# Performance work log

Measured on AMD Instinct MI355X. Metric: run time of the kernel, lower is better.

The kernel has to match this reference:

```python
import jax, jax.numpy as jnp
import numpy as np

DIM = 512
HEADS = 8
HEAD_DIM = DIM // HEADS
KS = 5


def setup_inputs() -> dict:
    key = jax.random.key(0)
    ks = jax.random.split(key, 6)
    B, H, W = 4, 128, 128
    N, C = H * W, DIM
    x = jax.random.normal(ks[0], (B, N, C), jnp.float32)
    Wq = jax.random.normal(ks[1], (C, C), jnp.float32) * 0.02
    bq = jnp.zeros((C,), jnp.float32)
    Wkv = jax.random.normal(ks[2], (2 * C, C), jnp.float32) * 0.02
    bkv = jnp.zeros((2 * C,), jnp.float32)
    Wp = jax.random.normal(ks[3], (C, C), jnp.float32) * 0.02
    bp = jnp.zeros((C,), jnp.float32)
    focusing_factor = jnp.ones((C,), jnp.float32) * 3.0
    scale = jnp.zeros((C,), jnp.float32)
    dwc_w = jax.random.normal(ks[4], (HEAD_DIM, 1, KS, KS), jnp.float32) * np.sqrt(2.0 / (KS * KS)).astype(np.float32)
    dwc_b = jnp.zeros((HEAD_DIM,), jnp.float32)
    return {"x": x, "Wq": Wq, "bq": bq, "Wkv": Wkv, "bkv": bkv, "Wp": Wp, "bp": bp,
            "focusing_factor": focusing_factor, "scale": scale, "dwc_w": dwc_w, "dwc_b": dwc_b,
            "H": H, "W": W}


def reference(x, Wq, bq, Wkv, bkv, Wp, bp, focusing_factor, scale, dwc_w, dwc_b, H, W):
    B, N, C = x.shape
    h, d = HEADS, C // HEADS
    q = x @ Wq.T + bq
    kv = x @ Wkv.T + bkv
    k, v = kv[..., :C], kv[..., C:]
    s = jax.nn.softplus(scale)
    q = (jax.nn.relu(q) + 1e-6) / s
    k = (jax.nn.relu(k) + 1e-6) / s
    q_norm = jnp.linalg.norm(q, axis=-1, keepdims=True)
    k_norm = jnp.linalg.norm(k, axis=-1, keepdims=True)
    q = q ** focusing_factor
    k = k ** focusing_factor
    q = q / jnp.linalg.norm(q, axis=-1, keepdims=True) * q_norm
    k = k / jnp.linalg.norm(k, axis=-1, keepdims=True) * k_norm
    # [B, h, N, d]
    q = q.reshape(B, N, h, d).transpose(0, 2, 1, 3)
    k = k.reshape(B, N, h, d).transpose(0, 2, 1, 3)
    v = v.reshape(B, N, h, d).transpose(0, 2, 1, 3)
    n = N
    k_mean = k.mean(axis=2)  # [B, h, d]
    z = 1.0 / (jnp.einsum('bhnd,bhd->bhn', q, k_mean) + 1e-6)  # [B, h, N]
    inv_sqrt_n = n ** (-0.5)
    kv_mat = jnp.einsum('bhnd,bhne->bhde', k * inv_sqrt_n, v * inv_sqrt_n)  # [B, h, d, d]
    attn = jnp.einsum('bhnd,bhde->bhne', q, kv_mat) * z[..., None]  # [B, h, N, d]
    x_attn = attn.transpose(0, 2, 1, 3).reshape(B, N, C)
    # depthwise conv branch on v, per (batch*head) image of shape [d, H, W]
    v_img = v.reshape(B * h, H, W, d).transpose(0, 3, 1, 2)
    pad = KS // 2
    conv = jax.lax.conv_general_dilated(v_img, dwc_w, (1, 1), [(pad, pad), (pad, pad)],
                                        feature_group_count=d,
                                        dimension_numbers=('NCHW', 'OIHW', 'NCHW'))
    conv = conv + dwc_b[None, :, None, None]
    x_conv = conv.reshape(B, C, N).transpose(0, 2, 1)
    return (x_attn + x_conv) @ Wp.T + bp
```

## Files before the change

### kernel.cpp

```cpp
#include <hip/hip_runtime.h>
#include <cstdio>

#define N_TOK 16384
#define CDIM  512

typedef unsigned short ushort_t;
typedef _Float16 f16;
typedef __attribute__((ext_vector_type(8))) _Float16 f16x8;
typedef __attribute__((ext_vector_type(4))) _Float16 f16x4;
typedef __attribute__((ext_vector_type(4))) float f32x4;

__device__ __forceinline__ float fast_pow(float x, float p) {
  return __builtin_amdgcn_exp2f(p * __builtin_amdgcn_logf(x));
}
__device__ __forceinline__ void gl_lds16(const void* g, void* l) {
  __builtin_amdgcn_global_load_lds((const __attribute__((address_space(1))) void*)g,
                                   (__attribute__((address_space(3))) void*)l, 16, 0, 0);
}
__device__ __forceinline__ int perm_col(int k, int r) {
  const int kg = k >> 5, c8 = (k >> 3) & 3, e = k & 7;
  return kg * 32 + ((c8 ^ ((r >> 1) & 3)) * 8) + e;
}

__global__ void zero_kernel(float* __restrict__ p, int n) {
  int i = blockIdx.x * blockDim.x + threadIdx.x;
  if (i < n) p[i] = 0.f;
}

__global__ void sp_kernel(const float* __restrict__ scale, float* __restrict__ inv_s) {
  int i = blockIdx.x * blockDim.x + threadIdx.x;
  if (i < 512) {
    float sc = scale[i];
    float s = (sc > 20.f) ? sc : log1pf(expf(sc));
    inv_s[i] = 1.0f / s;
  }
}

__global__ __launch_bounds__(256) void cvt_perm_kernel(const float* __restrict__ in,
                                                       f16* __restrict__ out, int n4) {
  int i = blockIdx.x * blockDim.x + threadIdx.x;
  const int stride = gridDim.x * blockDim.x;
  for (; i < n4; i += stride) {
    float4 v = ((const float4*)in)[i];
    const int r = i >> 7;
    const int f = i & 127;
    const int kg = f >> 3;
    const int c = (f >> 1) & 3;
    const int e = (f & 1) * 4;
    const int dst = r * 512 + kg * 32 + ((c ^ ((r >> 1) & 3)) * 8) + e;
    f16x4 h;
    h.x = (f16)v.x; h.y = (f16)v.y; h.z = (f16)v.z; h.w = (f16)v.w;
    *(f16x4*)&out[dst] = h;
  }
}

template <int OUT16>
__global__ __launch_bounds__(256, 4) void gemm_f16(const f16* __restrict__ A,
                                                   const f16* __restrict__ Bw,
                                                   const float* __restrict__ b1,
                                                   const float* __restrict__ b2,
                                                   float* __restrict__ C32,
                                                   f16* __restrict__ C16,
                                                   const int K, const int nY,
                                                   const int ncol1, const int ldc) {
  __shared__ __align__(16) f16 SMEM[16896];
  const int t = threadIdx.x;
  const int lane = t & 63;
  const int w = t >> 6;
  const int wr = w >> 1, wc = w & 1;

  const int id = blockIdx.x;
  const int xcd = id & 7;
  const int j = id >> 3;
  const int xpc = (int)(gridDim.x) / (nY * 8);
  const int xloc = j / nY;
  const int y = j - xloc * nY;
  const size_t bm = (size_t)(xcd * xpc + xloc) * 128;
  const int bn = y * 128;

  const int lr = lane & 15;
  const int ksl = lane >> 4;

  f32x4 acc[4][4] = {};

  auto stage = [&](int k0, int buf) {
    const int rsub = lane >> 2;
    const int csub = (lane & 3) * 8;
    const size_t ga = (bm + w * 32 + rsub) * (size_t)K + k0 + csub;
    const size_t gb = ((size_t)(bn + w * 32 + rsub)) * K + k0 + csub;
    f16* Ab = SMEM + buf * 4096;
    f16* Bb = SMEM + 8192 + buf * 4096;
    gl_lds16(A + ga,                   Ab + (w * 32) * 32);
    gl_lds16(A + ga + 16 * (size_t)K,  Ab + (w * 32 + 16) * 32);
    gl_lds16(Bw + gb,                  Bb + (w * 32) * 32);
    gl_lds16(Bw + gb + 16 * (size_t)K, Bb + (w * 32 + 16) * 32);
  };

  const int nsteps = K >> 5;
  stage(0, 0);
  for (int s = 0; s < nsteps; ++s) {
    const int buf = s & 1;
    __syncthreads();
    const f16* Ab = SMEM + buf * 4096;
    const f16* Bb = SMEM + 8192 + buf * 4096;
    f16x8 a[4], b[4];
#pragma unroll
    for (int i = 0; i < 4; ++i) {
      const int rA = wr * 64 + i * 16 + lr;
      a[i] = *(const f16x8*)&Ab[rA * 32 + ((ksl ^ ((rA >> 1) & 3)) * 8)];
      const int rB = wc * 64 + i * 16 + lr;
      b[i] = *(const f16x8*)&Bb[rB * 32 + ((ksl ^ ((rB >> 1) & 3)) * 8)];
    }
    if (s + 1 < nsteps) stage((s + 1) << 5, buf ^ 1);
#pragma unroll
    for (int mi = 0; mi < 4; ++mi)
#pragma unroll
      for (int ni = 0; ni < 4; ++ni)
        acc[mi][ni] = __builtin_amdgcn_mfma_f32_16x16x32_f16(a[mi], b[ni], acc[mi][ni], 0, 0, 0);
  }

  const int rg = (lane >> 4) << 2;
  if (OUT16) {
    __syncthreads();
#pragma unroll
    for (int ni = 0; ni < 4; ++ni) {
      const int cl = wc * 64 + ni * 16 + lr;
      const int cg = bn + cl;
      const float bs = (cg < ncol1) ? b1[cg] : b2[cg - ncol1];
#pragma unroll
      for (int mi = 0; mi < 4; ++mi)
#pragma unroll
        for (int j2 = 0; j2 < 4; ++j2)
          SMEM[(wr * 64 + mi * 16 + rg + j2) * 132 + cl] = (f16)(acc[mi][ni][j2] + bs);
    }
    __syncthreads();
#pragma unroll
    for (int i = 0; i < 8; ++i) {
      const int idx = i * 256 + t;
      const int rl = idx >> 4, ch = (idx & 15) * 8;
      *(f16x8*)&C16[(bm + rl) * (size_t)ldc + bn + ch] = *(const f16x8*)&SMEM[rl * 132 + ch];
    }
  } else {
#pragma unroll
    for (int ni = 0; ni < 4; ++ni) {
      const int col = bn + wc * 64 + ni * 16 + lr;
      const float bs = (col < ncol1) ? b1[col] : b2[col - ncol1];
#pragma unroll
      for (int mi = 0; mi < 4; ++mi) {
        float* Cp = C32 + (bm + wr * 64 + mi * 16 + rg) * (size_t)ldc + col;
#pragma unroll
        for (int j2 = 0; j2 < 4; ++j2)
          Cp[(size_t)j2 * ldc] = acc[mi][ni][j2] + bs;
      }
    }
  }
}

__global__ __launch_bounds__(256) void nonlin16_kernel(f16* __restrict__ qkv,
                                                       const float* __restrict__ inv_s,
                                                       const float* __restrict__ ff) {
  const int t = threadIdx.x, lane = t & 63, w = t >> 6;
  const int row = blockIdx.x * 4 + w;
  f16* qr = qkv + (size_t)row * 1536 + lane * 8;
  f16* kr = qr + 512;
  f16x8 qh = *(const f16x8*)qr;
  f16x8 kh = *(const f16x8*)kr;
  float is[8], fv[8];
  *(float4*)&is[0] = *(const float4*)(inv_s + lane * 8);
  *(float4*)&is[4] = *(const float4*)(inv_s + lane * 8 + 4);
  *(float4*)&fv[0] = *(const float4*)(ff + lane * 8);
  *(float4*)&fv[4] = *(const float4*)(ff + lane * 8 + 4);

  float qv[8], kval[8], sq = 0.f, sk = 0.f;
#pragma unroll
  for (int i = 0; i < 8; ++i) {
    qv[i] = (fmaxf((float)qh[i], 0.f) + 1e-6f) * is[i];
    kval[i] = (fmaxf((float)kh[i], 0.f) + 1e-6f) * is[i];
    sq += qv[i] * qv[i];
    sk += kval[i] * kval[i];
  }
#pragma unroll
  for (int off = 1; off < 64; off <<= 1) {
    sq += __shfl_xor(sq, off);
    sk += __shfl_xor(sk, off);
  }
  const float qn = sqrtf(sq), kn = sqrtf(sk);

  float pq[8], pk[8], sq2 = 0.f, sk2 = 0.f;
#pragma unroll
  for (int i = 0; i < 8; ++i) {
    pq[i] = fast_pow(qv[i], fv[i]);
    pk[i] = fast_pow(kval[i], fv[i]);
    sq2 += pq[i] * pq[i];
    sk2 += pk[i] * pk[i];
  }
#pragma unroll
  for (int off = 1; off < 64; off <<= 1) {
    sq2 += __shfl_xor(sq2, off);
    sk2 += __shfl_xor(sk2, off);
  }
  const float qs = qn / sqrtf(sq2), ks = kn / sqrtf(sk2);
  f16x8 qo, ko;
#pragma unroll
  for (int i = 0; i < 8; ++i) {
    qo[i] = (f16)(pq[i] * qs);
    ko[i] = (f16)(pk[i] * ks);
  }
  *(f16x8*)qr = qo;
  *(f16x8*)kr = ko;
}

__global__ __launch_bounds__(256, 4) void kvmat16_kernel(const f16* __restrict__ qkv,
                                                         float* __restrict__ kvm,
                                                         float* __restrict__ ksum) {
  __shared__ float tile[64 * 66];
  const int bh = blockIdx.y;
  const int b = bh >> 3, h = bh & 7;
  const int chunk = blockIdx.x;
  const int t = threadIdx.x, lane = t & 63, w = t >> 6;
  const int r0 = lane >> 3;
  const int c0 = lane & 7;
  float acc[8][8] = {};
  float kacc = 0.f;
  const size_t base = ((size_t)b * N_TOK + (size_t)chunk * 512 + w * 128) * 1536 + 512 + h * 64;
  const f16* kp = qkv + base + lane;
  const f16* vp = qkv + base + 512 + lane;

  float kcur = (float)kp[0], vcur = (float)vp[0];
  auto body = [&](float kc, float vc) {
    kacc += kc;
    float kk[8], vv[8];
#pragma unroll
    for (int i = 0; i < 8; ++i) {
      kk[i] = __shfl(kc, r0 + i * 8);
      vv[i] = __shfl(vc, c0 + i * 8);
    }
#pragma unroll
    for (int i = 0; i < 8; ++i)
#pragma unroll
      for (int j = 0; j < 8; ++j)
        acc[i][j] = fmaf(kk[i], vv[j], acc[i][j]);
  };
  for (int r = 0; r < 127; ++r) {
    const float knx = (float)kp[(size_t)(r + 1) * 1536];
    const float vnx = (float)vp[(size_t)(r + 1) * 1536];
    body(kcur, vcur);
    kcur = knx; vcur = vnx;
  }
  body(kcur, vcur);

  atomicAdd(&ksum[b * 512 + h * 64 + lane], kacc);

  for (int ww = 0; ww < 4; ++ww) {
    if (w == ww) {
#pragma unroll
      for (int i = 0; i < 8; ++i)
#pragma unroll
        for (int j = 0; j < 8; ++j) {
          const int a = (r0 + i * 8) * 66 + c0 + j * 8;
          tile[a] = (ww == 0) ? acc[i][j] : tile[a] + acc[i][j];
        }
    }
    __syncthreads();
  }
  const float scl = 1.0f / (float)N_TOK;
#pragma unroll
  for (int i = 0; i < 16; ++i) {
    const int idx = i * 256 + t;
    const int rr = idx >> 6, cc = idx & 63;
    atomicAdd(&kvm[(size_t)bh * 4096 + idx], tile[rr * 66 + cc] * scl);
  }
}

__global__ void cvt_kvmT_kernel(const float* __restrict__ kvm, f16* __restrict__ kvmT16) {
  const int bh = blockIdx.x, t = threadIdx.x;
#pragma unroll
  for (int i = 0; i < 16; ++i) {
    const int e = i * 256 + t;
    const int din = e >> 6, d = e & 63;
    const float v = kvm[(size_t)bh * 4096 + e];
    const int c = din >> 3, ce = din & 7;
    kvmT16[(size_t)bh * 4096 + d * 64 + ((c ^ (d & 7)) * 8) + ce] = (f16)v;
  }
}

__global__ __launch_bounds__(256, 4) void attn_mfma_kernel(const f16* __restrict__ qkv,
                                                           const f16* __restrict__ kvmT16,
                                                           const float* __restrict__ ksum,
                                                           f16* __restrict__ y16) {
  __shared__ __align__(16) f16 QS[128 * 64];
  __shared__ __align__(16) f16 KM[64 * 64];
  __shared__ float kms[64];
  __shared__ float zl[128];
  const int bh = blockIdx.y;
  const int b = bh >> 3, h = bh & 7;
  const int tok0 = blockIdx.x * 128;
  const int t = threadIdx.x, lane = t & 63, w = t >> 6;

#pragma unroll
  for (int i = 0; i < 4; ++i) {
    const int idx = i * 256 + t;
    const int row = idx >> 3, ch = idx & 7;
    const f16x8 v = *(const f16x8*)&qkv[((size_t)(b * N_TOK) + tok0 + row) * 1536 + h * 64 + ch * 8];
    *(f16x8*)&QS[row * 64 + ((ch ^ (row & 7)) * 8)] = v;
  }
#pragma unroll
  for (int i = 0; i < 2; ++i) {
    const int idx = i * 256 + t;
    *(f16x8*)&KM[idx * 8] = *(const f16x8*)&kvmT16[(size_t)bh * 4096 + idx * 8];
  }
  if (t < 64) kms[t] = ksum[b * 512 + h * 64 + t];
  __syncthreads();

  {
    const int tok = t >> 1;
    const int ch0 = (t & 1) * 4;
    float p = 0.f;
#pragma unroll
    for (int c = 0; c < 4; ++c) {
      const int ch = ch0 + c;
      const f16x8 hv = *(const f16x8*)&QS[tok * 64 + ((ch ^ (tok & 7)) * 8)];
#pragma unroll
      for (int e = 0; e < 8; ++e) p += (float)hv[e] * kms[ch * 8 + e];
    }
    p += __shfl_xor(p, 1);
    if ((t & 1) == 0) zl[tok] = 1.0f / (p * (1.0f / (float)N_TOK) + 1e-6f);
  }
  __syncthreads();

  const int lr = lane & 15, ksl = lane >> 4;
  f32x4 acc[2][4] = {};
#pragma unroll
  for (int s = 0; s < 2; ++s) {
    f16x8 a[2], bfr[4];
#pragma unroll
    for (int mi = 0; mi < 2; ++mi) {
      const int row = w * 32 + mi * 16 + lr;
      a[mi] = *(const f16x8*)&QS[row * 64 + (((s * 4 + ksl) ^ (row & 7)) * 8)];
    }
#pragma unroll
    for (int ni = 0; ni < 4; ++ni) {
      const int dr = ni * 16 + lr;
      bfr[ni] = *(const f16x8*)&KM[dr * 64 + (((s * 4 + ksl) ^ (dr & 7)) * 8)];
    }
#pragma unroll
    for (int mi = 0; mi < 2; ++mi)
#pragma unroll
      for (int ni = 0; ni < 4; ++ni)
        acc[mi][ni] = __builtin_amdgcn_mfma_f32_16x16x32_f16(a[mi], bfr[ni], acc[mi][ni], 0, 0, 0);
  }

  const int rg = (lane >> 4) << 2;
#pragma unroll
  for (int mi = 0; mi < 2; ++mi)
#pragma unroll
    for (int ni = 0; ni < 4; ++ni)
#pragma unroll
      for (int j2 = 0; j2 < 4; ++j2) {
        const int row = w * 32 + mi * 16 + rg + j2;
        const int dcol = ni * 16 + lr;
        const float val = acc[mi][ni][j2] * zl[row];
        const int r = (int)(b * N_TOK) + tok0 + row;
        y16[(size_t)r * 512 + perm_col(h * 64 + dcol, r)] = (f16)val;
      }
}

__global__ __launch_bounds__(256, 4) void conv_kernel(const f16* __restrict__ qkv,
                                                      f16* __restrict__ y16,
                                                      const float* __restrict__ wconv,
                                                      const float* __restrict__ bconv) {
  __shared__ float vt[20 * 20 * 16];
  const int zidx = blockIdx.z;
  const int bh = zidx >> 2, cq = zidx & 3;
  const int b = bh >> 3, h = bh & 7;
  const int c0 = cq * 16;
  const int tx0 = blockIdx.x * 16, ty0 = blockIdx.y * 16;
  const int t = threadIdx.x;
  const size_t vcol = 1024 + h * 64 + c0;
#pragma unroll
  for (int i = 0; i < 7; ++i) {
    const int idx = i * 256 + t;
    if (idx < 1600) {
      const int pix = idx >> 2, c4 = (idx & 3) * 4;
      const int lx = pix % 20, ly = pix / 20;
      const int gx = tx0 + lx - 2, gy = ty0 + ly - 2;
      float4 val = make_float4(0.f, 0.f, 0.f, 0.f);
      if ((unsigned)gx < 128u && (unsigned)gy < 128u) {
        f16x4 hv = *(const f16x4*)&qkv[((size_t)(b * N_TOK) + gy * 128 + gx) * 1536 + vcol + c4];
        val = make_float4((float)hv.x, (float)hv.y, (float)hv.z, (float)hv.w);
      }
      *(float4*)&vt[pix * 16 + c4] = val;
    }
  }
  const int c = t & 15;
  const int dd = c0 + c;
  float w[25];
#pragma unroll
  for (int k = 0; k < 25; ++k) w[k] = wconv[dd * 25 + k];
  const float bb = bconv[dd];
  __syncthreads();
  const int slot = t >> 4;
  const int col = h * 64 + dd;
  for (int i = 0; i < 16; ++i) {
    const int pix = i * 16 + slot;
    const int px = pix & 15, py = pix >> 4;
    float acc = bb;
#pragma unroll
    for (int ky = 0; ky < 5; ++ky)
#pragma unroll
      for (int kx = 0; kx < 5; ++kx)
        acc = fmaf(w[ky * 5 + kx], vt[((py + ky) * 20 + (px + kx)) * 16 + c], acc);
    const int r = (int)(b * N_TOK) + (ty0 + py) * 128 + (tx0 + px);
    f16* p = &y16[(size_t)r * 512 + perm_col(col, r)];
    *p = (f16)((float)*p + acc);
  }
}

extern "C" void kernel_launch(void* const* d_in, const int* in_sizes, int n_in,
                              void* d_out, int out_size, void* d_ws, size_t ws_size,
                              hipStream_t stream) {
  (void)n_in; (void)out_size;
  const float* x     = (const float*)d_in[0];
  const float* Wq    = (const float*)d_in[1];
  const float* bq    = (const float*)d_in[2];
  const float* Wkv   = (const float*)d_in[3];
  const float* bkv   = (const float*)d_in[4];
  const float* Wp    = (const float*)d_in[5];
  const float* bp    = (const float*)d_in[6];
  const float* ff    = (const float*)d_in[7];
  const float* scale = (const float*)d_in[8];
  const float* dwc_w = (const float*)d_in[9];
  const float* dwc_b = (const float*)d_in[10];

  const int B = in_sizes[0] / (N_TOK * CDIM);
  const int M = B * N_TOK;

  f16*   qkv16 = (f16*)d_ws;
  f16*   y16   = qkv16 + (size_t)M * 1536;
  float* ksum  = (float*)(y16 + (size_t)M * 512);
  float* kvm   = ksum + (size_t)B * 512;
  float* zscr  = kvm + (size_t)B * 8 * 4096;

  size_t need = ((size_t)M * 1536 + (size_t)B * 512 + (size_t)B * 8 * 4096 +
                 (size_t)B * 8 * N_TOK) * sizeof(float);
  if (ws_size < need) {
    fprintf(stderr, "kernel_launch: ws too small (%zu < %zu)\n", ws_size, need);
    return;
  }

  f16* x16    = (f16*)d_out;
  f16* wqkv16 = x16 + (size_t)M * 512;
  f16* wp16    = (f16*)zscr;
  float* inv_s = zscr + 131072;
  f16* kvmT16  = (f16*)(inv_s + 512);

  const int nsmall = B * 512 + B * 8 * 4096;
  zero_kernel<<<(nsmall + 255) / 256, 256, 0, stream>>>(ksum, nsmall);
  sp_kernel<<<2, 256, 0, stream>>>(scale, inv_s);
  cvt_perm_kernel<<<4096, 256, 0, stream>>>(x, x16, M * 512 / 4);
  cvt_perm_kernel<<<256, 256, 0, stream>>>(Wq, wqkv16, 512 * 512 / 4);
  cvt_perm_kernel<<<512, 256, 0, stream>>>(Wkv, wqkv16 + 512 * 512, 1024 * 512 / 4);
  cvt_perm_kernel<<<256, 256, 0, stream>>>(Wp, wp16, 512 * 512 / 4);

  gemm_f16<1><<<(M / 128) * 12, 256, 0, stream>>>(x16, wqkv16, bq, bkv,
                                                  nullptr, qkv16, CDIM, 12, 512, 1536);

  nonlin16_kernel<<<M / 4, 256, 0, stream>>>(qkv16, inv_s, ff);
  kvmat16_kernel<<<dim3(32, B * 8), 256, 0, stream>>>(qkv16, kvm, ksum);
  cvt_kvmT_kernel<<<B * 8, 256, 0, stream>>>(kvm, kvmT16);
  attn_mfma_kernel<<<dim3(N_TOK / 128, B * 8), 256, 0, stream>>>(qkv16, kvmT16, ksum, y16);
  conv_kernel<<<dim3(8, 8, B * 8 * 4), 256, 0, stream>>>(qkv16, y16, dwc_w, dwc_b);

  gemm_f16<0><<<(M / 128) * 4, 256, 0, stream>>>(y16, wp16, bp, bp,
                                                 (float*)d_out, nullptr, CDIM, 4, 512, 512);
}
```

Baseline: 505.2 us.

## Store per-row norm scales and recompute q/k nonlinearity in consumer kernels

The nonlinearity kernel no longer writes transformed q and k back to the qkv buffer. It only reads them and stores two per-row scale factors. The kv-matrix and attention kernels recompute relu, the power and the row scale on the fly from the raw projections. This removes the write-back of the q/k half of qkv, at the cost of extra transcendental work in the consumers and extra scale loads. A small priority bump around the MFMA loop is also added.

After: 513.0 us. No clear change (+1.5%).

```diff
diff --git a/kernel.cpp b/kernel.cpp
--- a/kernel.cpp
+++ b/kernel.cpp
@@ -156,13 +156,14 @@
   }
 }
 
-__global__ __launch_bounds__(256) void nonlin16_kernel(f16* __restrict__ qkv,
-                                                       const float* __restrict__ inv_s,
-                                                       const float* __restrict__ ff) {
+__global__ __launch_bounds__(256) void norm_kernel(const f16* __restrict__ qkv,
+                                                   const float* __restrict__ inv_s,
+                                                   const float* __restrict__ ff,
+                                                   float* __restrict__ rowscale) {
   const int t = threadIdx.x, lane = t & 63, w = t >> 6;
   const int row = blockIdx.x * 4 + w;
-  f16* qr = qkv + (size_t)row * 1536 + lane * 8;
-  f16* kr = qr + 512;
+  const f16* qr = qkv + (size_t)row * 1536 + lane * 8;
+  const f16* kr = qr + 512;
   f16x8 qh = *(const f16x8*)qr;
   f16x8 kh = *(const f16x8*)kr;
   float is[8], fv[8];
@@ -171,46 +172,35 @@
   *(float4*)&fv[0] = *(const float4*)(ff + lane * 8);
   *(float4*)&fv[4] = *(const float4*)(ff + lane * 8 + 4);
 
-  float qv[8], kval[8], sq = 0.f, sk = 0.f;
+  float sq = 0.f, sk = 0.f, sq2 = 0.f, sk2 = 0.f;
 #pragma unroll
   for (int i = 0; i < 8; ++i) {
-    qv[i] = (fmaxf((float)qh[i], 0.f) + 1e-6f) * is[i];
-    kval[i] = (fmaxf((float)kh[i], 0.f) + 1e-6f) * is[i];
-    sq += qv[i] * qv[i];
-    sk += kval[i] * kval[i];
+    const float qv = fmaf(fmaxf((float)qh[i], 0.f), is[i], 1e-6f * is[i]);
+    const float kv = fmaf(fmaxf((float)kh[i], 0.f), is[i], 1e-6f * is[i]);
+    sq += qv * qv;
+    sk += kv * kv;
+    const float pq = fast_pow(qv, fv[i]);
+    const float pk = fast_pow(kv, fv[i]);
+    sq2 += pq * pq;
+    sk2 += pk * pk;
   }
 #pragma unroll
   for (int off = 1; off < 64; off <<= 1) {
     sq += __shfl_xor(sq, off);
     sk += __shfl_xor(sk, off);
-  }
-  const float qn = sqrtf(sq), kn = sqrtf(sk);
-
-  float pq[8], pk[8], sq2 = 0.f, sk2 = 0.f;
-#pragma unroll
-  for (int i = 0; i < 8; ++i) {
-    pq[i] = fast_pow(qv[i], fv[i]);
-    pk[i] = fast_pow(kval[i], fv[i]);
-    sq2 += pq[i] * pq[i];
-    sk2 += pk[i] * pk[i];
-  }
-#pragma unroll
-  for (int off = 1; off < 64; off <<= 1) {
     sq2 += __shfl_xor(sq2, off);
     sk2 += __shfl_xor(sk2, off);
   }
-  const float qs = qn / sqrtf(sq2), ks = kn / sqrtf(sk2);
-  f16x8 qo, ko;
-#pragma unroll
-  for (int i = 0; i < 8; ++i) {
-    qo[i] = (f16)(pq[i] * qs);
-    ko[i] = (f16)(pk[i] * ks);
-  }
-  *(f16x8*)qr = qo;
-  *(f16x8*)kr = ko;
+  if (lane == 0) {
+    rowscale[(size_t)row * 2]     = sqrtf(sq) / sqrtf(sq2);
+    rowscale[(size_t)row * 2 + 1] = sqrtf(sk) / sqrtf(sk2);
+  }
 }
 
 __global__ __launch_bounds__(256, 4) void kvmat16_kernel(const f16* __restrict__ qkv,
+                                                         const float* __restrict__ inv_s,
+                                                         const float* __restrict__ ff,
+                                                         const float* __restrict__ rowscale,
                                                          float* __restrict__ kvm,
                                                          float* __restrict__ ksum) {
   __shared__ float tile[64 * 66];
@@ -220,14 +210,19 @@
   const int t = threadIdx.x, lane = t & 63, w = t >> 6;
   const int r0 = lane >> 3;
   const int c0 = lane & 7;
+  const int cg = h * 64 + lane;
+  const float is = inv_s[cg], fe = ff[cg], epsis = 1e-6f * is;
   float acc[8][8] = {};
   float kacc = 0.f;
-  const size_t base = ((size_t)b * N_TOK + (size_t)chunk * 512 + w * 128) * 1536 + 512 + h * 64;
+  const int row0 = b * N_TOK + chunk * 512 + w * 128;
+  const size_t base = (size_t)row0 * 1536 + 512 + h * 64;
   const f16* kp = qkv + base + lane;
   const f16* vp = qkv + base + 512 + lane;
 
   float kcur = (float)kp[0], vcur = (float)vp[0];
-  auto body = [&](float kc, float vc) {
+  float kscur = rowscale[(size_t)row0 * 2 + 1];
+  auto body = [&](float kraw, float vc, float ksc) {
+    const float kc = fast_pow(fmaf(fmaxf(kraw, 0.f), is, epsis), fe) * ksc;
     kacc += kc;
     float kk[8], vv[8];
 #pragma unroll
@@ -244,10 +239,11 @@
   for (int r = 0; r < 127; ++r) {
     const float knx = (float)kp[(size_t)(r + 1) * 1536];
     const float vnx = (float)vp[(size_t)(r + 1) * 1536];
-    body(kcur, vcur);
-    kcur = knx; vcur = vnx;
-  }
-  body(kcur, vcur);
+    const float ksnx = rowscale[(size_t)(row0 + r + 1) * 2 + 1];
+    body(kcur, vcur, kscur);
+    kcur = knx; vcur = vnx; kscur = ksnx;
+  }
+  body(kcur, vcur, kscur);
 
   atomicAdd(&ksum[b * 512 + h * 64 + lane], kacc);
 
@@ -287,6 +283,9 @@
 __global__ __launch_bounds__(256, 4) void attn_mfma_kernel(const f16* __restrict__ qkv,
                                                            const f16* __restrict__ kvmT16,
                                                            const float* __restrict__ ksum,
+                                                           const float* __restrict__ inv_s,
+                                                           const float* __restrict__ ff,
+                                                           const float* __restrict__ rowscale,
                                                            f16* __restrict__ y16) {
   __shared__ __align__(16) f16 QS[128 * 64];
   __shared__ __align__(16) f16 KM[64 * 64];
@@ -301,8 +300,22 @@
   for (int i = 0; i < 4; ++i) {
     const int idx = i * 256 + t;
     const int row = idx >> 3, ch = idx & 7;
-    const f16x8 v = *(const f16x8*)&qkv[((size_t)(b * N_TOK) + tok0 + row) * 1536 + h * 64 + ch * 8];
-    *(f16x8*)&QS[row * 64 + ((ch ^ (row & 7)) * 8)] = v;
+    const int gr = b * N_TOK + tok0 + row;
+    const f16x8 v = *(const f16x8*)&qkv[(size_t)gr * 1536 + h * 64 + ch * 8];
+    const float qsc = rowscale[(size_t)gr * 2];
+    const int ci = h * 64 + ch * 8;
+    float isv[8], fvv[8];
+    *(float4*)&isv[0] = *(const float4*)&inv_s[ci];
+    *(float4*)&isv[4] = *(const float4*)&inv_s[ci + 4];
+    *(float4*)&fvv[0] = *(const float4*)&ff[ci];
+    *(float4*)&fvv[4] = *(const float4*)&ff[ci + 4];
+    f16x8 o;
+#pragma unroll
+    for (int e = 0; e < 8; ++e) {
+      const float q_ = fmaf(fmaxf((float)v[e], 0.f), isv[e], 1e-6f * isv[e]);
+      o[e] = (f16)(fast_pow(q_, fvv[e]) * qsc);
+    }
+    *(f16x8*)&QS[row * 64 + ((ch ^ (row & 7)) * 8)] = o;
   }
 #pragma unroll
   for (int i = 0; i < 2; ++i) {
@@ -330,6 +343,7 @@
 
   const int lr = lane & 15, ksl = lane >> 4;
   f32x4 acc[2][4] = {};
+  __builtin_amdgcn_s_setprio(1);
 #pragma unroll
   for (int s = 0; s < 2; ++s) {
     f16x8 a[2], bfr[4];
@@ -349,6 +363,7 @@
       for (int ni = 0; ni < 4; ++ni)
         acc[mi][ni] = __builtin_amdgcn_mfma_f32_16x16x32_f16(a[mi], bfr[ni], acc[mi][ni], 0, 0, 0);
   }
+  __builtin_amdgcn_s_setprio(0);
 
   const int rg = (lane >> 4) << 2;
 #pragma unroll
@@ -450,9 +465,10 @@
 
   f16* x16    = (f16*)d_out;
   f16* wqkv16 = x16 + (size_t)M * 512;
-  f16* wp16    = (f16*)zscr;
-  float* inv_s = zscr + 131072;
-  f16* kvmT16  = (f16*)(inv_s + 512);
+  f16* wp16      = (f16*)zscr;
+  float* inv_s   = zscr + 131072;
+  f16* kvmT16    = (f16*)(inv_s + 512);
+  float* rowscale = (float*)(kvmT16 + 131072);
 
   const int nsmall = B * 512 + B * 8 * 4096;
   zero_kernel<<<(nsmall + 255) / 256, 256, 0, stream>>>(ksum, nsmall);
@@ -465,10 +481,11 @@
   gemm_f16<1><<<(M / 128) * 12, 256, 0, stream>>>(x16, wqkv16, bq, bkv,
                                                   nullptr, qkv16, CDIM, 12, 512, 1536);
 
-  nonlin16_kernel<<<M / 4, 256, 0, stream>>>(qkv16, inv_s, ff);
-  kvmat16_kernel<<<dim3(32, B * 8), 256, 0, stream>>>(qkv16, kvm, ksum);
+  norm_kernel<<<M / 4, 256, 0, stream>>>(qkv16, inv_s, ff, rowscale);
+  kvmat16_kernel<<<dim3(32, B * 8), 256, 0, stream>>>(qkv16, inv_s, ff, rowscale, kvm, ksum);
   cvt_kvmT_kernel<<<B * 8, 256, 0, stream>>>(kvm, kvmT16);
-  attn_mfma_kernel<<<dim3(N_TOK / 128, B * 8), 256, 0, stream>>>(qkv16, kvmT16, ksum, y16);
+  attn_mfma_kernel<<<dim3(N_TOK / 128, B * 8), 256, 0, stream>>>(qkv16, kvmT16, ksum,
+                                                                 inv_s, ff, rowscale, y16);
   conv_kernel<<<dim3(8, 8, B * 8 * 4), 256, 0, stream>>>(qkv16, y16, dwc_w, dwc_b);
 
   gemm_f16<0><<<(M / 128) * 4, 256, 0, stream>>>(y16, wp16, bp, bp,
```

## Compute K^T V reduction with MFMA via LDS-transposed tiles

Applied to the files above, without the earlier changes.

Replaces the scalar FMA outer-product kernel for the per-head K^T V matrix with an MFMA version. Each wave loads 32-token slices of K and V with vector loads, transposes them into LDS, and issues 16x16x32 f16 MFMAs, also summing K rows from the fragments. This removes the shuffle-heavy scalar loop and narrow per-element global loads, at the cost of LDS transposes with possible bank conflicts. It also raises wave priority around the MFMA loop in the attention kernel.

After: 438.4 us. 13.2% less time.

```diff
diff --git a/kernel.cpp b/kernel.cpp
--- a/kernel.cpp
+++ b/kernel.cpp
@@ -210,56 +210,84 @@
   *(f16x8*)kr = ko;
 }
 
-__global__ __launch_bounds__(256, 4) void kvmat16_kernel(const f16* __restrict__ qkv,
+__global__ __launch_bounds__(256) void kvmat_mfma_kernel(const f16* __restrict__ qkv,
                                                          float* __restrict__ kvm,
                                                          float* __restrict__ ksum) {
-  __shared__ float tile[64 * 66];
+  __shared__ __align__(16) f16 ST[20480];
   const int bh = blockIdx.y;
   const int b = bh >> 3, h = bh & 7;
   const int chunk = blockIdx.x;
   const int t = threadIdx.x, lane = t & 63, w = t >> 6;
-  const int r0 = lane >> 3;
-  const int c0 = lane & 7;
-  float acc[8][8] = {};
-  float kacc = 0.f;
-  const size_t base = ((size_t)b * N_TOK + (size_t)chunk * 512 + w * 128) * 1536 + 512 + h * 64;
-  const f16* kp = qkv + base + lane;
-  const f16* vp = qkv + base + 512 + lane;
-
-  float kcur = (float)kp[0], vcur = (float)vp[0];
-  auto body = [&](float kc, float vc) {
-    kacc += kc;
-    float kk[8], vv[8];
-#pragma unroll
-    for (int i = 0; i < 8; ++i) {
-      kk[i] = __shfl(kc, r0 + i * 8);
-      vv[i] = __shfl(vc, c0 + i * 8);
-    }
-#pragma unroll
-    for (int i = 0; i < 8; ++i)
-#pragma unroll
-      for (int j = 0; j < 8; ++j)
-        acc[i][j] = fmaf(kk[i], vv[j], acc[i][j]);
-  };
-  for (int r = 0; r < 127; ++r) {
-    const float knx = (float)kp[(size_t)(r + 1) * 1536];
-    const float vnx = (float)vp[(size_t)(r + 1) * 1536];
-    body(kcur, vcur);
-    kcur = knx; vcur = vnx;
-  }
-  body(kcur, vcur);
-
-  atomicAdd(&ksum[b * 512 + h * 64 + lane], kacc);
-
+  f16* kT = ST + w * 5120;
+  f16* vT = kT + 2560;
+  const int tok = lane & 31, half = lane >> 5;
+  const int lr = lane & 15, ksl = lane >> 4;
+  f32x4 acc[4][4] = {};
+  float kacc[4] = {0.f, 0.f, 0.f, 0.f};
+  const int rowbase = b * N_TOK + chunk * 512 + w * 128;
+
+  for (int s = 0; s < 4; ++s) {
+    const size_t g = (size_t)(rowbase + s * 32 + tok) * 1536 + 512 + h * 64 + half * 32;
+    f16x8 kr[4], vr[4];
+#pragma unroll
+    for (int j = 0; j < 4; ++j) {
+      kr[j] = *(const f16x8*)&qkv[g + j * 8];
+      vr[j] = *(const f16x8*)&qkv[g + 512 + j * 8];
+    }
+#pragma unroll
+    for (int j = 0; j < 4; ++j)
+#pragma unroll
+      for (int e = 0; e < 8; ++e) {
+        const int ch = half * 32 + j * 8 + e;
+        kT[ch * 40 + tok] = kr[j][e];
+        vT[ch * 40 + tok] = vr[j][e];
+      }
+    f16x8 a[4], bv[4];
+#pragma unroll
+    for (int mi = 0; mi < 4; ++mi)
+      a[mi] = *(const f16x8*)&kT[(mi * 16 + lr) * 40 + ksl * 8];
+#pragma unroll
+    for (int ni = 0; ni < 4; ++ni)
+      bv[ni] = *(const f16x8*)&vT[(ni * 16 + lr) * 40 + ksl * 8];
+#pragma unroll
+    for (int mi = 0; mi < 4; ++mi) {
+      float s8 = 0.f;
+#pragma unroll
+      for (int e = 0; e < 8; ++e) s8 += (float)a[mi][e];
+      kacc[mi] += s8;
+    }
+#pragma unroll
+    for (int mi = 0; mi < 4; ++mi)
+#pragma unroll
+      for (int ni = 0; ni < 4; ++ni)
+        acc[mi][ni] = __builtin_amdgcn_mfma_f32_16x16x32_f16(a[mi], bv[ni], acc[mi][ni], 0, 0, 0);
+  }
+
+#pragma unroll
+  for (int mi = 0; mi < 4; ++mi) {
+    kacc[mi] += __shfl_xor(kacc[mi], 16);
+    kacc[mi] += __shfl_xor(kacc[mi], 32);
+  }
+  if (ksl == 0) {
+#pragma unroll
+    for (int mi = 0; mi < 4; ++mi)
+      atomicAdd(&ksum[b * 512 + h * 64 + mi * 16 + lr], kacc[mi]);
+  }
+
+  float* tile = (float*)ST;
+  const int rg = (lane >> 4) << 2;
+  __syncthreads();
   for (int ww = 0; ww < 4; ++ww) {
     if (w == ww) {
 #pragma unroll
-      for (int i = 0; i < 8; ++i)
-#pragma unroll
-        for (int j = 0; j < 8; ++j) {
-          const int a = (r0 + i * 8) * 66 + c0 + j * 8;
-          tile[a] = (ww == 0) ? acc[i][j] : tile[a] + acc[i][j];
-        }
+      for (int mi = 0; mi < 4; ++mi)
+#pragma unroll
+        for (int ni = 0; ni < 4; ++ni)
+#pragma unroll
+          for (int j2 = 0; j2 < 4; ++j2) {
+            const int aidx = (mi * 16 + rg + j2) * 66 + ni * 16 + lr;
+            tile[aidx] = (ww == 0) ? acc[mi][ni][j2] : tile[aidx] + acc[mi][ni][j2];
+          }
     }
     __syncthreads();
   }
@@ -330,6 +358,7 @@
 
   const int lr = lane & 15, ksl = lane >> 4;
   f32x4 acc[2][4] = {};
+  __builtin_amdgcn_s_setprio(1);
 #pragma unroll
   for (int s = 0; s < 2; ++s) {
     f16x8 a[2], bfr[4];
@@ -349,6 +378,7 @@
       for (int ni = 0; ni < 4; ++ni)
         acc[mi][ni] = __builtin_amdgcn_mfma_f32_16x16x32_f16(a[mi], bfr[ni], acc[mi][ni], 0, 0, 0);
   }
+  __builtin_amdgcn_s_setprio(0);
 
   const int rg = (lane >> 4) << 2;
 #pragma unroll
@@ -466,7 +496,7 @@
                                                   nullptr, qkv16, CDIM, 12, 512, 1536);
 
   nonlin16_kernel<<<M / 4, 256, 0, stream>>>(qkv16, inv_s, ff);
-  kvmat16_kernel<<<dim3(32, B * 8), 256, 0, stream>>>(qkv16, kvm, ksum);
+  kvmat_mfma_kernel<<<dim3(32, B * 8), 256, 0, stream>>>(qkv16, kvm, ksum);
   cvt_kvmT_kernel<<<B * 8, 256, 0, stream>>>(kvm, kvmT16);
   attn_mfma_kernel<<<dim3(N_TOK / 128, B * 8), 256, 0, stream>>>(qkv16, kvmT16, ksum, y16);
   conv_kernel<<<dim3(8, 8, B * 8 * 4), 256, 0, stream>>>(qkv16, y16, dwc_w, dwc_b);
```
